# Kernel optimization log

Measured on AMD Instinct MI355X. Metric: run time of the kernel, lower is better.

The kernel has to match this reference:

```python
import jax, jax.numpy as jnp
import numpy as np

B, S, IN, OUT, GS = 4, 2048, 4096, 4096, 256
NG = IN // GS  # number of groups per output channel


def setup_inputs() -> dict:
    key = jax.random.key(0)
    k1, k2, k3, k4 = jax.random.split(key, 4)
    x = jax.random.normal(k1, (B, S, IN), dtype=jnp.float32)
    # int4 codes stored in int8: values in [-8, 7]
    weight_int8 = jax.random.randint(k2, (OUT, IN), -8, 8, dtype=jnp.int32).astype(jnp.int8)
    scales = jax.random.uniform(k3, (OUT, NG), dtype=jnp.float32, minval=0.001, maxval=0.02)
    # zero points stored in scales_precision (float), integer-valued in int4 range
    zeros = jax.random.randint(k4, (OUT, NG), -8, 8, dtype=jnp.int32).astype(jnp.float32)
    return {"x": x, "weight_int8": weight_int8, "scales": scales, "zeros": zeros,
            "group_size": GS}


def per_token_dynamic_quant(x):
    """Asymmetric per-token int8 quantize -> dequantize (torchao decomposed ops)."""
    qmin, qmax = -128.0, 127.0
    mn = jnp.minimum(jnp.min(x, axis=-1, keepdims=True), 0.0)
    mx = jnp.maximum(jnp.max(x, axis=-1, keepdims=True), 0.0)
    eps = jnp.finfo(jnp.float32).eps
    scale = jnp.maximum((mx - mn) / (qmax - qmin), eps)
    # choose zero point minimizing error at whichever end is larger
    zp = jnp.where((qmin + mn / scale) + (qmax + mx / scale) > 0,
                   qmin - mn / scale, qmax - mx / scale)
    zp = jnp.clip(jnp.round(zp), qmin, qmax)
    q = jnp.clip(jnp.round(x / scale) + zp, qmin, qmax)
    return (q - zp) * scale


def dequant_per_channel_group(w_int8, scales, zeros, group_size):
    O, I = w_int8.shape
    g = I // group_size
    w = w_int8.reshape(O, g, group_size).astype(jnp.float32)
    w_dq = (w - zeros[:, :, None]) * scales[:, :, None]
    return w_dq.reshape(O, I)


def reference(x, weight_int8, scales, zeros, group_size):
    xq = per_token_dynamic_quant(x.astype(jnp.float32))
    w_dq = dequant_per_channel_group(weight_int8, scales, zeros, group_size)
    # F.linear: x @ w_dq.T  -> [B, S, OUT]
    return jnp.einsum('bsi,oi->bso', xq, w_dq)
```

## Files before the change

### kernel.cpp

```cpp
#include <hip/hip_runtime.h>
#include <hip/hip_bf16.h>
#include <stdint.h>

#define T_   8192
#define IN_  4096
#define OUT_ 4096
#define GS_  256
#define NG_  16

#define BM 128
#define BN 128
#define BK 128
#define KT (IN_ / BK)

typedef int   v4i __attribute__((ext_vector_type(4)));
typedef float f4  __attribute__((ext_vector_type(4)));

__device__ __forceinline__ void gload16(const void* g, void* l) {
  __builtin_amdgcn_global_load_lds(
      (const __attribute__((address_space(1))) void*)g,
      (__attribute__((address_space(3))) void*)l, 16, 0, 0);
}

__global__ __launch_bounds__(256) void quant_kernel(
    const float* __restrict__ x, int8_t* __restrict__ q,
    float* __restrict__ tscale, float* __restrict__ tzp) {
  const int t = blockIdx.x;
  const int tid = threadIdx.x;
  const float* xr = x + (size_t)t * IN_ + tid * 16;
  float vals[16];
  {
    f4 v0 = *(const f4*)(xr);
    f4 v1 = *(const f4*)(xr + 4);
    f4 v2 = *(const f4*)(xr + 8);
    f4 v3 = *(const f4*)(xr + 12);
#pragma unroll
    for (int i = 0; i < 4; ++i) {
      vals[i] = v0[i]; vals[4 + i] = v1[i]; vals[8 + i] = v2[i]; vals[12 + i] = v3[i];
    }
  }
  float mn = 0.f, mx = 0.f;
#pragma unroll
  for (int i = 0; i < 16; ++i) { mn = fminf(mn, vals[i]); mx = fmaxf(mx, vals[i]); }
#pragma unroll
  for (int off = 32; off > 0; off >>= 1) {
    mn = fminf(mn, __shfl_xor(mn, off));
    mx = fmaxf(mx, __shfl_xor(mx, off));
  }
  __shared__ float smn[4], smx[4];
  if ((tid & 63) == 0) { smn[tid >> 6] = mn; smx[tid >> 6] = mx; }
  __syncthreads();
  mn = fminf(fminf(smn[0], smn[1]), fminf(smn[2], smn[3]));
  mx = fmaxf(fmaxf(smx[0], smx[1]), fmaxf(smx[2], smx[3]));

  const float eps = 1.1920928955078125e-7f;
  float scale = fmaxf((mx - mn) / 255.0f, eps);
  float rmn = mn / scale;
  float rmx = mx / scale;
  float zp0 = ((-128.0f + rmn) + (127.0f + rmx) > 0.0f) ? (-128.0f - rmn)
                                                        : (127.0f - rmx);
  float zp = fminf(fmaxf(rintf(zp0), -128.0f), 127.0f);
  if (tid == 0) { tscale[t] = scale; tzp[t] = zp; }

  const float inv = 1.0f / scale;
  v4i packed;
#pragma unroll
  for (int w = 0; w < 4; ++w) {
    int word = 0;
#pragma unroll
    for (int e = 0; e < 4; ++e) {
      float qf = rintf(vals[w * 4 + e] * inv) + zp;
      qf = fminf(fmaxf(qf, -128.0f), 127.0f);
      int qi = (int)qf;
      word |= (qi & 0xff) << (8 * e);
    }
    packed[w] = word;
  }
  *(v4i*)(q + (size_t)t * IN_ + tid * 16) = packed;
}

__global__ __launch_bounds__(256) void wprep_kernel(
    const int* __restrict__ w, const float* __restrict__ scales,
    const float* __restrict__ zeros, int8_t* __restrict__ wq,
    float* __restrict__ c1) {
  const int o = blockIdx.x;
  const int tid = threadIdx.x;
  const int g = tid >> 4;
  const int* wr = w + (size_t)o * IN_ + tid * 16;
  const int zi = (int)zeros[o * NG_ + g];
  int ssum = 0;
  v4i packed;
#pragma unroll
  for (int blk = 0; blk < 4; ++blk) {
    v4i ww = *(const v4i*)(wr + blk * 4);
    int word = 0;
#pragma unroll
    for (int e = 0; e < 4; ++e) {
      int wp = ww[e] - zi;
      ssum += wp;
      word |= (wp & 0xff) << (8 * e);
    }
    packed[blk] = word;
  }
  *(v4i*)(wq + (size_t)o * IN_ + tid * 16) = packed;
  ssum += __shfl_xor(ssum, 1);
  ssum += __shfl_xor(ssum, 2);
  ssum += __shfl_xor(ssum, 4);
  ssum += __shfl_xor(ssum, 8);
  __shared__ float part[NG_];
  if ((tid & 15) == 0) part[g] = scales[o * NG_ + g] * (float)ssum;
  __syncthreads();
  if (tid == 0) {
    float s = 0.f;
#pragma unroll
    for (int i = 0; i < NG_; ++i) s += part[i];
    c1[o] = s;
  }
}

__global__ __launch_bounds__(256, 2) void gemm_kernel(
    const int8_t* __restrict__ q, const int8_t* __restrict__ wq,
    const float* __restrict__ scales, const float* __restrict__ tscale,
    const float* __restrict__ tzp, const float* __restrict__ c1,
    float* __restrict__ out) {
  __shared__ int8_t As[2][BM * BK];
  __shared__ int8_t Bs[2][BN * BK];
  __shared__ float sSc[NG_ * BN];

  const int tid = threadIdx.x;
  const int lane = tid & 63;
  const int wid = tid >> 6;
  const int R0 = blockIdx.y * BM;
  const int C0 = blockIdx.x * BN;

#pragma unroll
  for (int e = 0; e < 8; ++e) {
    int idx = tid + e * 256;
    int oc = idx >> 4, g = idx & 15;
    sSc[g * BN + oc] = scales[(size_t)(C0 + oc) * NG_ + g];
  }

  const int rA = tid >> 3;
  const int cswz = ((tid & 7) ^ (rA & 7)) * 16;
  const int8_t* gA = q + (size_t)(R0 + rA) * IN_ + cswz;
  const int8_t* gB = wq + (size_t)(C0 + rA) * IN_ + cswz;

  const int wm = (wid >> 1) * 64;
  const int wn = (wid & 1) * 64;
  const int lm = lane & 15;
  const int quad = lane >> 4;
  const int o0 = ((quad ^ (lm & 7)) * 16);
  const int aRow = (wm + lm) * BK;
  const int bRow = (wn + lm) * BK;

  v4i acci[4][4];
  float accf[4][4][4];
#pragma unroll
  for (int i = 0; i < 4; ++i)
#pragma unroll
    for (int j = 0; j < 4; ++j) {
      acci[i][j] = (v4i){0, 0, 0, 0};
#pragma unroll
      for (int r = 0; r < 4; ++r) accf[i][j][r] = 0.f;
    }

#pragma unroll
  for (int i = 0; i < 4; ++i) {
    gload16(gA + (size_t)(i * 32) * IN_, &As[0][i * 4096 + tid * 16]);
    gload16(gB + (size_t)(i * 32) * IN_, &Bs[0][i * 4096 + tid * 16]);
  }
  __syncthreads();

  int cur = 0;
  for (int kt = 0; kt < KT; ++kt) {
    if (kt + 1 < KT) {
      const size_t koff = (size_t)(kt + 1) * BK;
#pragma unroll
      for (int i = 0; i < 4; ++i) {
        gload16(gA + koff + (size_t)(i * 32) * IN_,
                &As[cur ^ 1][i * 4096 + tid * 16]);
        gload16(gB + koff + (size_t)(i * 32) * IN_,
                &Bs[cur ^ 1][i * 4096 + tid * 16]);
      }
    }

#pragma unroll
    for (int ks = 0; ks < 2; ++ks) {
      const int co = o0 ^ (ks * 64);
      v4i af[4], bf[4];
#pragma unroll
      for (int i = 0; i < 4; ++i)
        af[i] = *(const v4i*)&As[cur][aRow + i * (16 * BK) + co];
#pragma unroll
      for (int j = 0; j < 4; ++j)
        bf[j] = *(const v4i*)&Bs[cur][bRow + j * (16 * BK) + co];
#pragma unroll
      for (int i = 0; i < 4; ++i)
#pragma unroll
        for (int j = 0; j < 4; ++j)
          acci[i][j] =
              __builtin_amdgcn_mfma_i32_16x16x64_i8(af[i], bf[j], acci[i][j], 0, 0, 0);
    }

    if (kt & 1) {
      const int g = kt >> 1;
      float sj[4];
#pragma unroll
      for (int j = 0; j < 4; ++j) sj[j] = sSc[g * BN + wn + j * 16 + lm];
#pragma unroll
      for (int i = 0; i < 4; ++i)
#pragma unroll
        for (int j = 0; j < 4; ++j) {
#pragma unroll
          for (int r = 0; r < 4; ++r)
            accf[i][j][r] += sj[j] * (float)acci[i][j][r];
          acci[i][j] = (v4i){0, 0, 0, 0};
        }
    }

    __syncthreads();
    cur ^= 1;
  }

  float cj[4];
#pragma unroll
  for (int j = 0; j < 4; ++j) cj[j] = c1[C0 + wn + j * 16 + lm];
#pragma unroll
  for (int i = 0; i < 4; ++i) {
#pragma unroll
    for (int r = 0; r < 4; ++r) {
      const int row = R0 + wm + i * 16 + quad * 4 + r;
      const float tsc = tscale[row];
      const float tz = tzp[row];
#pragma unroll
      for (int j = 0; j < 4; ++j) {
        const int col = C0 + wn + j * 16 + lm;
        out[(size_t)row * OUT_ + col] = tsc * (accf[i][j][r] - tz * cj[j]);
      }
    }
  }
}

extern "C" void kernel_launch(void* const* d_in, const int* in_sizes, int n_in,
                              void* d_out, int out_size, void* d_ws, size_t ws_size,
                              hipStream_t stream) {
  const float* x = (const float*)d_in[0];
  const int* w = (const int*)d_in[1];
  const float* scales = (const float*)d_in[2];
  const float* zeros = (const float*)d_in[3];

  uint8_t* ws = (uint8_t*)d_ws;
  int8_t* q = (int8_t*)ws;
  int8_t* wq = (int8_t*)(ws + 33554432);
  float* tscale = (float*)(ws + 33554432 + 16777216);
  float* tzp = (float*)(ws + 33554432 + 16777216 + 32768);
  float* c1 = (float*)(ws + 33554432 + 16777216 + 65536);
  float* out = (float*)d_out;

  hipLaunchKernelGGL(quant_kernel, dim3(T_), dim3(256), 0, stream, x, q, tscale, tzp);
  hipLaunchKernelGGL(wprep_kernel, dim3(OUT_), dim3(256), 0, stream, w, scales, zeros, wq, c1);
  hipLaunchKernelGGL(gemm_kernel, dim3(OUT_ / BN, T_ / BM), dim3(256), 0, stream,
                     q, wq, scales, tscale, tzp, c1, out);
}
```

Measured before the change: 433.5 us.

## Load weight operand directly from global into registers, bypassing shared memory

The GEMM no longer stages the weight tile through double-buffered LDS. Each wave reads its B fragments straight from global memory into registers every K step, and only the activation tile still goes through LDS. This halves LDS use, and the launch-bounds occupancy hint is raised from 2 to 4 blocks per CU. The B global loads are not prefetched, so their latency sits directly in front of the MFMAs. The tighter register budget also risks spilling the integer and float accumulators.

```diff
diff --git a/kernel.cpp b/kernel.cpp
--- a/kernel.cpp
+++ b/kernel.cpp
@@ -118,13 +118,12 @@
   }
 }
 
-__global__ __launch_bounds__(256, 2) void gemm_kernel(
+__global__ __launch_bounds__(256, 4) void gemm_kernel(
     const int8_t* __restrict__ q, const int8_t* __restrict__ wq,
     const float* __restrict__ scales, const float* __restrict__ tscale,
     const float* __restrict__ tzp, const float* __restrict__ c1,
     float* __restrict__ out) {
   __shared__ int8_t As[2][BM * BK];
-  __shared__ int8_t Bs[2][BN * BK];
   __shared__ float sSc[NG_ * BN];
 
   const int tid = threadIdx.x;
@@ -143,7 +142,6 @@
   const int rA = tid >> 3;
   const int cswz = ((tid & 7) ^ (rA & 7)) * 16;
   const int8_t* gA = q + (size_t)(R0 + rA) * IN_ + cswz;
-  const int8_t* gB = wq + (size_t)(C0 + rA) * IN_ + cswz;
 
   const int wm = (wid >> 1) * 64;
   const int wn = (wid & 1) * 64;
@@ -151,7 +149,8 @@
   const int quad = lane >> 4;
   const int o0 = ((quad ^ (lm & 7)) * 16);
   const int aRow = (wm + lm) * BK;
-  const int bRow = (wn + lm) * BK;
+
+  const int8_t* bBase = wq + (size_t)(C0 + wn + lm) * IN_ + quad * 16;
 
   v4i acci[4][4];
   float accf[4][4][4];
@@ -165,10 +164,8 @@
     }
 
 #pragma unroll
-  for (int i = 0; i < 4; ++i) {
+  for (int i = 0; i < 4; ++i)
     gload16(gA + (size_t)(i * 32) * IN_, &As[0][i * 4096 + tid * 16]);
-    gload16(gB + (size_t)(i * 32) * IN_, &Bs[0][i * 4096 + tid * 16]);
-  }
   __syncthreads();
 
   int cur = 0;
@@ -176,30 +173,43 @@
     if (kt + 1 < KT) {
       const size_t koff = (size_t)(kt + 1) * BK;
 #pragma unroll
-      for (int i = 0; i < 4; ++i) {
+      for (int i = 0; i < 4; ++i)
         gload16(gA + koff + (size_t)(i * 32) * IN_,
                 &As[cur ^ 1][i * 4096 + tid * 16]);
-        gload16(gB + koff + (size_t)(i * 32) * IN_,
-                &Bs[cur ^ 1][i * 4096 + tid * 16]);
-      }
-    }
-
-#pragma unroll
-    for (int ks = 0; ks < 2; ++ks) {
-      const int co = o0 ^ (ks * 64);
-      v4i af[4], bf[4];
-#pragma unroll
-      for (int i = 0; i < 4; ++i)
-        af[i] = *(const v4i*)&As[cur][aRow + i * (16 * BK) + co];
-#pragma unroll
-      for (int j = 0; j < 4; ++j)
-        bf[j] = *(const v4i*)&Bs[cur][bRow + j * (16 * BK) + co];
+    }
+
+    const int8_t* bk = bBase + (size_t)kt * BK;
+    v4i bf0[4], bf1[4];
+#pragma unroll
+    for (int j = 0; j < 4; ++j) {
+      bf0[j] = *(const v4i*)(bk + (size_t)j * (16 * IN_));
+      bf1[j] = *(const v4i*)(bk + (size_t)j * (16 * IN_) + 64);
+    }
+
+    {
+      v4i af[4];
+#pragma unroll
+      for (int i = 0; i < 4; ++i)
+        af[i] = *(const v4i*)&As[cur][aRow + i * (16 * BK) + o0];
 #pragma unroll
       for (int i = 0; i < 4; ++i)
 #pragma unroll
         for (int j = 0; j < 4; ++j)
           acci[i][j] =
-              __builtin_amdgcn_mfma_i32_16x16x64_i8(af[i], bf[j], acci[i][j], 0, 0, 0);
+              __builtin_amdgcn_mfma_i32_16x16x64_i8(af[i], bf0[j], acci[i][j], 0, 0, 0);
+    }
+    {
+      const int co = o0 ^ 64;
+      v4i af[4];
+#pragma unroll
+      for (int i = 0; i < 4; ++i)
+        af[i] = *(const v4i*)&As[cur][aRow + i * (16 * BK) + co];
+#pragma unroll
+      for (int i = 0; i < 4; ++i)
+#pragma unroll
+        for (int j = 0; j < 4; ++j)
+          acci[i][j] =
+              __builtin_amdgcn_mfma_i32_16x16x64_i8(af[i], bf1[j], acci[i][j], 0, 0, 0);
     }
 
     if (kt & 1) {
```

After: 885.5 us. 2.04x slower.
